# Optimization experiments

Hardware: AMD Instinct MI355X
Metric: run time of the kernel (lower is better)

The kernel has to match this reference:

```python
import jax, jax.numpy as jnp
import numpy as np

PATCH_SIZE = 14.0
PIXEL_THRESHOLD = 5.0


def setup_inputs() -> dict:
    key = jax.random.key(0)
    k1, k2, k3, k4, k5 = jax.random.split(key, 5)
    B, N = 32, 1024
    src_pts = jax.random.uniform(k1, (B, N, 2), dtype=jnp.float32) * 32.0  # patch coords
    tar_pts = jax.random.uniform(k2, (B, N, 2), dtype=jnp.float32) * 32.0
    scores = jax.random.uniform(k3, (B, N), dtype=jnp.float32)
    relScale = 0.5 + jax.random.uniform(k4, (B, N), dtype=jnp.float32)  # positive scales
    theta = jax.random.uniform(k5, (B, N), dtype=jnp.float32) * 2.0 * np.pi
    relInplane = jnp.stack([jnp.cos(theta), jnp.sin(theta)], axis=-1)  # (B,N,2) cos,sin
    return {"src_pts": src_pts, "tar_pts": tar_pts, "scores": scores,
            "relScale": relScale, "relInplane": relInplane}


def _ransac_single(src, tar, score, scale, inplane):
    # src, tar: (N,2); score, scale: (N,); inplane: (N,2) = (cos, sin)
    N = src.shape[0]
    valid = src[:, 0] != -1.0  # (N,) sentinel mask from original forward
    s = src * PATCH_SIZE
    t = tar * PATCH_SIZE
    c, si = inplane[:, 0], inplane[:, 1]
    # R = [[c, -s], [s, c]] per candidate -> (N,2,2)
    R = jnp.stack([jnp.stack([c, -si], -1), jnp.stack([si, c], -1)], -2)
    A = scale[:, None, None] * R                          # (N,2,2) linear part
    trans = t - jnp.einsum('nij,nj->ni', A, s)            # (N,2) translation so A@s_n + t_n == t_n
    # candidate n applied to every point m (leave-one-out handled by masking diag)
    pred = jnp.einsum('nij,mj->nmi', A, s) + trans[:, None, :]   # (N,N,2)
    err = jnp.linalg.norm(pred - t[None, :, :], axis=-1)          # (N,N)
    not_self = ~jnp.eye(N, dtype=bool)
    inlier = (err <= PIXEL_THRESHOLD) & valid[None, :] & not_self  # (N,N)
    score_inl = jnp.sum(inlier * score[None, :], axis=1)           # (N,)
    score_inl = jnp.where(valid, score_inl, -1.0)
    best = jnp.argmax(score_inl)
    failed = score_inl[best] == 0.0
    M = (jnp.eye(3, dtype=src.dtype)
         .at[:2, :2].set(A[best])
         .at[:2, 2].set(trans[best]))
    # pack inliers of best candidate to the front (original index order preserved)
    inl = inlier[best]                                   # (N,) bool
    order = jnp.argsort(jnp.where(inl, 0, 1), stable=True)
    cnt = jnp.sum(inl)
    keep = jnp.arange(N) < cnt
    out_src = jnp.where(keep[:, None], src[order], -1.0)
    out_tar = jnp.where(keep[:, None], tar[order], -1.0)
    out_sc = jnp.where(keep, score[order], 0.0)
    return M, failed, out_src, out_tar, out_sc


def reference(src_pts, tar_pts, scores, relScale, relInplane):
    Ms, failed, inl_src, inl_tar, inl_sc = jax.vmap(_ransac_single)(
        src_pts, tar_pts, scores, relScale, relInplane)
    return Ms, failed, inl_src, inl_tar, inl_sc
```

## Files before the change

kernel.cpp:

```cpp
#include <hip/hip_runtime.h>

constexpr int BB = 32;
constexpr int NN = 1024;
constexpr int TPB = 512;
constexpr int WAVES = 8;
constexpr int GH = 256;
constexpr int MQ = 256;
constexpr int ITERS = MQ / WAVES;
#define PATCH 14.0f
#define THRSQ 25.0f

__global__ __launch_bounds__(TPB, 3) void ransac_score_kernel(
    const float* __restrict__ src, const float* __restrict__ tar,
    const float* __restrict__ scores, const float* __restrict__ relScale,
    const float* __restrict__ relInplane, float* __restrict__ score_part)
{
#pragma clang fp contract(off)
    const int bid  = blockIdx.x;
    const int q    = bid & 3;
    const int g    = (bid >> 2) & 3;
    const int b    = bid >> 4;
    const int tid  = threadIdx.x;
    const int wave = tid >> 6;
    const int lane = tid & 63;

    __shared__ float4 pts[MQ];
    __shared__ float  sc[MQ];
    __shared__ float  partial[WAVES][GH];

    const float2* src2 = (const float2*)src + (size_t)b * NN;
    const float2* tar2 = (const float2*)tar + (size_t)b * NN;
    const float*  scb  = scores + (size_t)b * NN;
    const int mOff = q * MQ;

    if (tid < MQ) {
        float2 s = src2[mOff + tid];
        float2 t = tar2[mOff + tid];
        pts[tid] = make_float4(s.x * PATCH, s.y * PATCH, t.x * PATCH, t.y * PATCH);
        sc[tid]  = (s.x != -1.0f) ? scb[mOff + tid] : 0.0f;
    }

    const size_t nb = (size_t)b * NN;
    float a00[4], a01[4], a10[4], a11[4], trx[4], trY[4];
#pragma unroll
    for (int h = 0; h < 4; ++h) {
        const int n = g * GH + h * 64 + lane;
        const float sv  = relScale[nb + n];
        const float2 ip = ((const float2*)relInplane)[nb + n];
        float2 s = src2[n], t = tar2[n];
        a00[h] = sv * ip.x;  a01[h] = sv * (-ip.y);
        a10[h] = sv * ip.y;  a11[h] = sv * ip.x;
        const float Px = s.x * PATCH, Py = s.y * PATCH;
        const float Tx = t.x * PATCH, Ty = t.y * PATCH;
        trx[h] = Tx - (a00[h] * Px + a01[h] * Py);
        trY[h] = Ty - (a10[h] * Px + a11[h] * Py);
    }

    __syncthreads();

    float acc[4] = {0.0f, 0.0f, 0.0f, 0.0f};
    const int mBeg = wave * ITERS;
#pragma unroll 4
    for (int mm = 0; mm < ITERS; ++mm) {
        const float4 qp = pts[mBeg + mm];
        const float  w  = sc[mBeg + mm];
#pragma unroll
        for (int h = 0; h < 4; ++h) {
            float px = __builtin_fmaf(a00[h], qp.x, __builtin_fmaf(a01[h], qp.y, trx[h]));
            float py = __builtin_fmaf(a10[h], qp.x, __builtin_fmaf(a11[h], qp.y, trY[h]));
            float dx = px - qp.z, dy = py - qp.w;
            float e2 = __builtin_fmaf(dx, dx, dy * dy);
            acc[h] += (e2 <= THRSQ) ? w : 0.0f;
        }
    }
#pragma unroll
    for (int h = 0; h < 4; ++h) partial[wave][h * 64 + lane] = acc[h];
    __syncthreads();

    if (tid < GH) {
        float p = 0.0f;
#pragma unroll
        for (int w = 0; w < WAVES; ++w) p += partial[w][tid];
        if (g == q) p -= sc[tid];
        score_part[((size_t)q * BB + b) * NN + g * GH + tid] = p;
    }
}

__global__ __launch_bounds__(1024) void ransac_select_kernel(
    const float* __restrict__ src, const float* __restrict__ tar,
    const float* __restrict__ scores, const float* __restrict__ relScale,
    const float* __restrict__ relInplane,
    const float* __restrict__ score_part, float* __restrict__ out)
{
#pragma clang fp contract(off)
    const int b = blockIdx.x;
    const int tid = threadIdx.x;
    const int lane = tid & 63;
    const int wave = tid >> 6;

    __shared__ float wvalSh[16];
    __shared__ int   widxSh[16];
    __shared__ float prm[6];
    __shared__ int   bestIdxSh;
    __shared__ float bestValSh;
    __shared__ int   wcnt[16], wbase[16];
    __shared__ float osx[NN], osy[NN], otx[NN], oty[NN], osc[NN];

    const size_t gm = (size_t)b * NN + tid;
    const float2 s2 = ((const float2*)src)[gm];
    const float2 t2 = ((const float2*)tar)[gm];
    const float scin = scores[gm];

    float val;
    {
        float p = score_part[(size_t)b * NN + tid]
                + score_part[((size_t)BB + b) * NN + tid]
                + score_part[((size_t)2 * BB + b) * NN + tid]
                + score_part[((size_t)3 * BB + b) * NN + tid];
        val = (s2.x != -1.0f) ? p : -1.0f;
    }
    int idx = tid;

    for (int d = 1; d < 64; d <<= 1) {
        float ov = __shfl_xor(val, d);
        int   oi = __shfl_xor(idx, d);
        if (ov > val || (ov == val && oi < idx)) { val = ov; idx = oi; }
    }
    if (lane == 0) { wvalSh[wave] = val; widxSh[wave] = idx; }
    __syncthreads();
    if (tid < 64) {
        float v = (tid < 16) ? wvalSh[tid] : -1e30f;
        int   i = (tid < 16) ? widxSh[tid] : 0x7fffffff;
        for (int d = 1; d < 16; d <<= 1) {
            float ov = __shfl_xor(v, d);
            int   oi = __shfl_xor(i, d);
            if (ov > v || (ov == v && oi < i)) { v = ov; i = oi; }
        }
        if (tid == 0) { bestIdxSh = i; bestValSh = v; }
    }
    __syncthreads();
    const int best = bestIdxSh;

    if (tid == 0) {
        size_t gi = (size_t)b * NN + best;
        float scale = relScale[gi];
        float c  = relInplane[gi * 2];
        float si = relInplane[gi * 2 + 1];
        float a00 = scale * c;
        float a01 = scale * (-si);
        float a10 = scale * si;
        float a11 = scale * c;
        float snx = src[gi * 2] * PATCH, sny = src[gi * 2 + 1] * PATCH;
        float tnx = tar[gi * 2] * PATCH, tny = tar[gi * 2 + 1] * PATCH;
        float trx = tnx - (a00 * snx + a01 * sny);
        float trY = tny - (a10 * snx + a11 * sny);
        prm[0] = a00; prm[1] = a01; prm[2] = a10; prm[3] = a11; prm[4] = trx; prm[5] = trY;

        float* M = out + (size_t)b * 9;
        M[0] = a00; M[1] = a01; M[2] = trx;
        M[3] = a10; M[4] = a11; M[5] = trY;
        M[6] = 0.0f; M[7] = 0.0f; M[8] = 1.0f;
        out[(size_t)BB * 9 + b] = (bestValSh == 0.0f) ? 1.0f : 0.0f;
    }
    __syncthreads();

    float sx = s2.x * PATCH, sy = s2.y * PATCH;
    float tx = t2.x * PATCH, ty = t2.y * PATCH;
    float px = prm[0] * sx + prm[1] * sy + prm[4];
    float py = prm[2] * sx + prm[3] * sy + prm[5];
    float dx = px - tx, dy = py - ty;
    bool flag = (dx * dx + dy * dy <= THRSQ) && (s2.x != -1.0f) && (tid != best);

    unsigned long long mask = __ballot(flag);
    int posInWave = __popcll(mask & ((1ULL << lane) - 1ULL));
    if (lane == 0) wcnt[wave] = __popcll(mask);
    __syncthreads();
    if (tid < 16) {
        int s = 0;
        for (int i = 0; i < tid; ++i) s += wcnt[i];
        wbase[tid] = s;
    }
    __syncthreads();
    int pos = wbase[wave] + posInWave;

    osx[tid] = -1.0f; osy[tid] = -1.0f;
    otx[tid] = -1.0f; oty[tid] = -1.0f;
    osc[tid] = 0.0f;
    __syncthreads();
    if (flag) {
        osx[pos] = s2.x; osy[pos] = s2.y;
        otx[pos] = t2.x; oty[pos] = t2.y;
        osc[pos] = scin;
    }
    __syncthreads();

    const size_t O_SRC = (size_t)BB * 9 + BB;
    const size_t O_TAR = O_SRC + (size_t)BB * NN * 2;
    const size_t O_SC  = O_TAR + (size_t)BB * NN * 2;
    out[O_SRC + gm * 2]     = osx[tid];
    out[O_SRC + gm * 2 + 1] = osy[tid];
    out[O_TAR + gm * 2]     = otx[tid];
    out[O_TAR + gm * 2 + 1] = oty[tid];
    out[O_SC  + gm]         = osc[tid];
}

extern "C" void kernel_launch(void* const* d_in, const int* in_sizes, int n_in,
                              void* d_out, int out_size, void* d_ws, size_t ws_size,
                              hipStream_t stream) {
    const float* src        = (const float*)d_in[0];
    const float* tar        = (const float*)d_in[1];
    const float* scores     = (const float*)d_in[2];
    const float* relScale   = (const float*)d_in[3];
    const float* relInplane = (const float*)d_in[4];
    float* out = (float*)d_out;
    float* score_part = (float*)d_ws;

    ransac_score_kernel<<<BB * 4 * 4, TPB, 0, stream>>>(
        src, tar, scores, relScale, relInplane, score_part);
    ransac_select_kernel<<<BB, NN, 0, stream>>>(
        src, tar, scores, relScale, relInplane, score_part, out);
}
```

Baseline: 19.18 us.

## Precompute hypothesis params in separate kernel and exploit rotation symmetry in scoring

Adds a kernel that computes each candidate's similarity-transform parameters (a00, a01, translation) once into workspace, so the score kernel loads one float4 instead of recomputing from four inputs in all 4 q-blocks. The score loop uses the rotation structure (a10=-a01, a11=a00) to drop two registers per candidate. It also replaces the select-based threshold accumulate with a copysign/fmax form. The cost is an extra kernel launch and a global round trip on a workload that only takes microseconds.

```diff
diff --git a/kernel.cpp b/kernel.cpp
--- a/kernel.cpp
+++ b/kernel.cpp
@@ -10,10 +10,32 @@
 #define PATCH 14.0f
 #define THRSQ 25.0f
 
+__global__ __launch_bounds__(256) void ransac_params_kernel(
+    const float* __restrict__ src, const float* __restrict__ tar,
+    const float* __restrict__ relScale, const float* __restrict__ relInplane,
+    float4* __restrict__ hyp)
+{
+#pragma clang fp contract(off)
+    const size_t i = (size_t)blockIdx.x * 256 + threadIdx.x;
+    const float sv  = relScale[i];
+    const float2 ip = ((const float2*)relInplane)[i];
+    const float2 s  = ((const float2*)src)[i];
+    const float2 t  = ((const float2*)tar)[i];
+    const float a00 = sv * ip.x;
+    const float a01 = sv * (-ip.y);
+    const float a10 = sv * ip.y;
+    const float a11 = sv * ip.x;
+    const float Px = s.x * PATCH, Py = s.y * PATCH;
+    const float Tx = t.x * PATCH, Ty = t.y * PATCH;
+    const float trx = Tx - (a00 * Px + a01 * Py);
+    const float trY = Ty - (a10 * Px + a11 * Py);
+    hyp[i] = make_float4(a00, a01, trx, trY);
+}
+
 __global__ __launch_bounds__(TPB, 3) void ransac_score_kernel(
     const float* __restrict__ src, const float* __restrict__ tar,
-    const float* __restrict__ scores, const float* __restrict__ relScale,
-    const float* __restrict__ relInplane, float* __restrict__ score_part)
+    const float* __restrict__ scores, const float4* __restrict__ hyp,
+    float* __restrict__ score_part)
 {
 #pragma clang fp contract(off)
     const int bid  = blockIdx.x;
@@ -40,20 +62,12 @@
         sc[tid]  = (s.x != -1.0f) ? scb[mOff + tid] : 0.0f;
     }
 
-    const size_t nb = (size_t)b * NN;
-    float a00[4], a01[4], a10[4], a11[4], trx[4], trY[4];
+    const float4* hypb = hyp + (size_t)b * NN + g * GH;
+    float a00[4], a01[4], trx[4], trY[4];
 #pragma unroll
     for (int h = 0; h < 4; ++h) {
-        const int n = g * GH + h * 64 + lane;
-        const float sv  = relScale[nb + n];
-        const float2 ip = ((const float2*)relInplane)[nb + n];
-        float2 s = src2[n], t = tar2[n];
-        a00[h] = sv * ip.x;  a01[h] = sv * (-ip.y);
-        a10[h] = sv * ip.y;  a11[h] = sv * ip.x;
-        const float Px = s.x * PATCH, Py = s.y * PATCH;
-        const float Tx = t.x * PATCH, Ty = t.y * PATCH;
-        trx[h] = Tx - (a00[h] * Px + a01[h] * Py);
-        trY[h] = Ty - (a10[h] * Px + a11[h] * Py);
+        float4 hp = hypb[h * 64 + lane];
+        a00[h] = hp.x; a01[h] = hp.y; trx[h] = hp.z; trY[h] = hp.w;
     }
 
     __syncthreads();
@@ -67,10 +81,10 @@
 #pragma unroll
         for (int h = 0; h < 4; ++h) {
             float px = __builtin_fmaf(a00[h], qp.x, __builtin_fmaf(a01[h], qp.y, trx[h]));
-            float py = __builtin_fmaf(a10[h], qp.x, __builtin_fmaf(a11[h], qp.y, trY[h]));
+            float py = __builtin_fmaf(-a01[h], qp.x, __builtin_fmaf(a00[h], qp.y, trY[h]));
             float dx = px - qp.z, dy = py - qp.w;
             float e2 = __builtin_fmaf(dx, dx, dy * dy);
-            acc[h] += (e2 <= THRSQ) ? w : 0.0f;
+            acc[h] += fmaxf(0.0f, __builtin_copysignf(w, THRSQ - e2));
         }
     }
 #pragma unroll
@@ -214,9 +228,12 @@
     const float* relInplane = (const float*)d_in[4];
     float* out = (float*)d_out;
     float* score_part = (float*)d_ws;
-
+    float4* hyp = (float4*)((char*)d_ws + 4u * BB * NN * sizeof(float));
+
+    ransac_params_kernel<<<(BB * NN) / 256, 256, 0, stream>>>(
+        src, tar, relScale, relInplane, hyp);
     ransac_score_kernel<<<BB * 4 * 4, TPB, 0, stream>>>(
-        src, tar, scores, relScale, relInplane, score_part);
+        src, tar, scores, hyp, score_part);
     ransac_select_kernel<<<BB, NN, 0, stream>>>(
         src, tar, scores, relScale, relInplane, score_part, out);
 }
```

New measurement: 24.75 us. +29.0%, slower.
